# Kernel optimization log

Measured on AMD Instinct MI355X. Metric: run time of the kernel, lower is better.

## Reference

```python
import jax, jax.numpy as jnp
import numpy as np

DIM = 1024
HEADS = 16
SEQ = 1024
BATCH = 4
SCALE = (DIM // HEADS) ** -0.5


def setup_inputs() -> dict:
    key = jax.random.key(0)
    ks = jax.random.split(key, 5)
    x = jax.random.normal(ks[0], (BATCH, SEQ, DIM), dtype=jnp.float32)
    # Linear weights stored [in, out]; y = x @ W + b (math-equivalent to torch Linear)
    w_qkv = jax.random.normal(ks[1], (DIM, 3 * DIM), dtype=jnp.float32) * (DIM ** -0.5)
    b_qkv = jnp.zeros((3 * DIM,), dtype=jnp.float32)
    w_proj = jax.random.normal(ks[2], (DIM, DIM), dtype=jnp.float32) * (DIM ** -0.5)
    b_proj = jnp.zeros((DIM,), dtype=jnp.float32)
    rel_table = jax.random.normal(ks[3], (2 * SEQ - 1, HEADS), dtype=jnp.float32) * 0.02
    coords = jnp.arange(SEQ)
    rel_index = (coords[:, None] - coords[None, :] + SEQ - 1).astype(jnp.int32)  # [N, N]
    return {"x": x, "w_qkv": w_qkv, "b_qkv": b_qkv, "w_proj": w_proj,
            "b_proj": b_proj, "rel_table": rel_table, "rel_index": rel_index}


def reference(x, w_qkv, b_qkv, w_proj, b_proj, rel_table, rel_index):
    B, N, C = x.shape
    H = HEADS
    hd = C // H
    qkv = (x @ w_qkv + b_qkv).reshape(B, N, 3, H, hd).transpose(2, 0, 3, 1, 4)  # [3,B,H,N,hd]
    q, k, v = qkv[0] * SCALE, qkv[1], qkv[2]
    attn = jnp.einsum('bhqe,bhke->bhqk', q, k)                 # [B,H,N,N]
    bias = rel_table[rel_index]                                 # [N,N,H] gather
    attn = attn + bias.transpose(2, 0, 1)[None]                 # add [1,H,N,N]
    attn = jax.nn.softmax(attn, axis=-1)
    # Faithful to the original einsum 'bnqk,bnqe->bnqe' (contracts k over attn only)
    out = jnp.einsum('bnqk,bnqe->bnqe', attn, v)                # [B,H,N,hd]
    out = out.transpose(0, 2, 1, 3).reshape(B, N, C)
    return out @ w_proj + b_proj
```

## Files before the change

kernel.cpp:

```cpp
#include <hip/hip_runtime.h>


#define DIMC 1024
#define MTOT 4096

__device__ __forceinline__ unsigned short f2bf(float f) {
  unsigned u = __float_as_uint(f);
  u += 0x7FFFu + ((u >> 16) & 1u);
  return (unsigned short)(u >> 16);
}

typedef __attribute__((ext_vector_type(8))) short short8;
typedef __attribute__((ext_vector_type(4))) float floatx4;

__device__ __forceinline__ void async_copy16(const unsigned short* g, unsigned short* l) {
  __builtin_amdgcn_global_load_lds(
      (const __attribute__((address_space(1))) unsigned int*)g,
      (__attribute__((address_space(3))) unsigned int*)l,
      16, 0, 0);
}

__global__ void cast_bf16_kernel(const float* __restrict__ in,
                                 unsigned short* __restrict__ out) {
  int i = (blockIdx.x * 256 + threadIdx.x) * 4;
  float4 f = *(const float4*)(in + i);
  ushort4 o;
  o.x = f2bf(f.x); o.y = f2bf(f.y); o.z = f2bf(f.z); o.w = f2bf(f.w);
  *(ushort4*)(out + i) = o;
}

__global__ void cast_slice_kernel(const float* __restrict__ in, int stride,
                                  int col0, unsigned short* __restrict__ out) {
  int i4 = blockIdx.x * 256 + threadIdx.x;
  int r = i4 >> 8;
  int c = (i4 & 255) * 4;
  float4 f = *(const float4*)(in + (size_t)r * stride + col0 + c);
  ushort4 o;
  o.x = f2bf(f.x); o.y = f2bf(f.y); o.z = f2bf(f.z); o.w = f2bf(f.w);
  *(ushort4*)(out + (size_t)r * DIMC + c) = o;
}

__global__ void transpose_cast_kernel(const float* __restrict__ in, int stride,
                                      int col0, unsigned short* __restrict__ out) {
  __shared__ float tile[32][33];
  const int t = threadIdx.x;
  const int tx = t & 31, ty = t >> 5;
  const int bx = blockIdx.x, by = blockIdx.y;
#pragma unroll
  for (int r = 0; r < 4; ++r) {
    int kl = ty + r * 8;
    tile[kl][tx] = in[(size_t)(by * 32 + kl) * stride + col0 + bx * 32 + tx];
  }
  __syncthreads();
#pragma unroll
  for (int r = 0; r < 4; ++r) {
    int nl = ty + r * 8;
    out[(size_t)(bx * 32 + nl) * DIMC + by * 32 + tx] = f2bf(tile[tx][nl]);
  }
}

__global__ void bias_partial_kernel(const float* __restrict__ b_v,
                                    const float* __restrict__ w_proj,
                                    float* __restrict__ b_c) {
  __shared__ float red[256];
  const int t = threadIdx.x;
  const int lane = t & 63, q = t >> 6;
  const int n = blockIdx.x * 64 + lane;
  const int j0 = blockIdx.y * 128 + q * 32;
  float s = 0.f;
#pragma unroll
  for (int i = 0; i < 32; ++i)
    s += b_v[j0 + i] * w_proj[(size_t)(j0 + i) * DIMC + n];
  red[t] = s;
  __syncthreads();
  if (q == 0) atomicAdd(&b_c[n], red[t] + red[t + 64] + red[t + 128] + red[t + 192]);
}

template <bool BF16_OUT>
__global__ __launch_bounds__(256, 2) void gemm_bt_kernel(
    const unsigned short* __restrict__ A,
    const unsigned short* __restrict__ Bt,
    const float* __restrict__ bias,
    const float* __restrict__ bias2,
    void* __restrict__ Cout, int M, int N, int K) {
  __shared__ __align__(16) unsigned short As[64 * 64];
  __shared__ __align__(16) unsigned short Bs[128 * 64];
  const int tid = threadIdx.x;
  const int wv = tid >> 6;
  const int lane = tid & 63;
  const int m0 = blockIdx.y * 64;
  const int n0 = blockIdx.x * 128;

  floatx4 acc[4][2] = {};

  const int srow = tid >> 3;
  const int skc = (tid & 7) ^ (srow & 7);
  const unsigned short* Ag0 = A + (size_t)(m0 + srow) * K + skc * 8;
  const unsigned short* Ag1 = A + (size_t)(m0 + 32 + srow) * K + skc * 8;
  const unsigned short* Bg0 = Bt + (size_t)(n0 + srow) * K + skc * 8;
  const unsigned short* Bg1 = Bt + (size_t)(n0 + 32 + srow) * K + skc * 8;
  const unsigned short* Bg2 = Bt + (size_t)(n0 + 64 + srow) * K + skc * 8;
  const unsigned short* Bg3 = Bt + (size_t)(n0 + 96 + srow) * K + skc * 8;
  unsigned short* AsW0 = As + (0 * 256 + wv * 64) * 8;
  unsigned short* AsW1 = As + (1 * 256 + wv * 64) * 8;
  unsigned short* BsW0 = Bs + (0 * 256 + wv * 64) * 8;
  unsigned short* BsW1 = Bs + (1 * 256 + wv * 64) * 8;
  unsigned short* BsW2 = Bs + (2 * 256 + wv * 64) * 8;
  unsigned short* BsW3 = Bs + (3 * 256 + wv * 64) * 8;

  const int lr = lane & 15;
  const int qr = lane >> 4;
  const int lx = lr & 7;

  for (int k0 = 0; k0 < K; k0 += 64) {
    async_copy16(Ag0 + k0, AsW0);
    async_copy16(Ag1 + k0, AsW1);
    async_copy16(Bg0 + k0, BsW0);
    async_copy16(Bg1 + k0, BsW1);
    async_copy16(Bg2 + k0, BsW2);
    async_copy16(Bg3 + k0, BsW3);
    __syncthreads();

    short8 a[2][4], b[2][2];
#pragma unroll
    for (int s = 0; s < 2; ++s) {
      const int kphys = ((s * 4 + qr) ^ lx) * 8;
#pragma unroll
      for (int mi = 0; mi < 4; ++mi)
        a[s][mi] = *(const short8*)(As + (mi * 16 + lr) * 64 + kphys);
#pragma unroll
      for (int ni = 0; ni < 2; ++ni)
        b[s][ni] = *(const short8*)(Bs + (wv * 32 + ni * 16 + lr) * 64 + kphys);
    }
#pragma unroll
    for (int s = 0; s < 2; ++s)
#pragma unroll
      for (int mi = 0; mi < 4; ++mi)
#pragma unroll
        for (int ni = 0; ni < 2; ++ni)
          acc[mi][ni] = __builtin_amdgcn_mfma_f32_16x16x32_bf16(a[s][mi], b[s][ni],
                                                                acc[mi][ni], 0, 0, 0);
    __syncthreads();
  }

#pragma unroll
  for (int mi = 0; mi < 4; ++mi) {
#pragma unroll
    for (int ni = 0; ni < 2; ++ni) {
      const int col = n0 + wv * 32 + ni * 16 + lr;
      float bv = 0.0f;
      if (bias)  bv += bias[col];
      if (bias2) bv += bias2[col];
#pragma unroll
      for (int r = 0; r < 4; ++r) {
        const int row = m0 + mi * 16 + qr * 4 + r;
        const float val = acc[mi][ni][r] + bv;
        if (BF16_OUT)
          ((unsigned short*)Cout)[(size_t)row * N + col] = f2bf(val);
        else
          ((float*)Cout)[(size_t)row * N + col] = val;
      }
    }
  }
}

extern "C" void kernel_launch(void* const* d_in, const int* in_sizes, int n_in,
                              void* d_out, int out_size, void* d_ws, size_t ws_size,
                              hipStream_t stream) {
  const float* x      = (const float*)d_in[0];
  const float* w_qkv  = (const float*)d_in[1];
  const float* b_qkv  = (const float*)d_in[2];
  const float* w_proj = (const float*)d_in[3];
  const float* b_proj = (const float*)d_in[4];
  float* out = (float*)d_out;

  char* ws = (char*)d_ws;
  unsigned short* xb  = (unsigned short*)(ws);
  unsigned short* WpT = (unsigned short*)(ws + (size_t)(8u << 20));
  unsigned short* Wvb = (unsigned short*)(ws + (size_t)(10u << 20));
  unsigned short* WcT = (unsigned short*)(ws + (size_t)(12u << 20));
  float*          b_c = (float*)(ws + (size_t)(14u << 20));

  cast_bf16_kernel<<<(MTOT * DIMC) / (256 * 4), 256, 0, stream>>>(x, xb);
  transpose_cast_kernel<<<dim3(32, 32), 256, 0, stream>>>(w_proj, DIMC, 0, WpT);
  cast_slice_kernel<<<(DIMC * DIMC) / (256 * 4), 256, 0, stream>>>(w_qkv, 3 * DIMC, 2 * DIMC, Wvb);
  hipMemsetAsync(b_c, 0, DIMC * sizeof(float), stream);
  bias_partial_kernel<<<dim3(16, 8), 256, 0, stream>>>(b_qkv + 2 * DIMC, w_proj, b_c);
  gemm_bt_kernel<true><<<dim3(DIMC / 128, DIMC / 64), 256, 0, stream>>>(
      WpT, Wvb, nullptr, nullptr, WcT, DIMC, DIMC, DIMC);
  gemm_bt_kernel<false><<<dim3(DIMC / 128, MTOT / 64), 256, 0, stream>>>(
      xb, WcT, b_c, b_proj, out, MTOT, DIMC, DIMC);
}
```

Before: 132.3 us.

## Fuse weight prep kernels and retile GEMMs with block swizzle

Merges the w_proj transpose-cast, the V-slice cast and the folded-bias reduction into one prep kernel, cutting three launches down to one. The GEMM is templated on tile size. The weight-fold GEMM now runs 64x64 tiles (256 blocks, more CU coverage), and the main GEMM runs 128x128 tiles with a 2x2 wave layout and a grouped block swizzle for L2 reuse. Larger tiles raise register pressure and leave only 256 blocks in the main GEMM, which may underfill the GPU.

```diff
diff --git a/kernel.cpp b/kernel.cpp
--- a/kernel.cpp
+++ b/kernel.cpp
@@ -29,19 +29,12 @@
   *(ushort4*)(out + i) = o;
 }
 
-__global__ void cast_slice_kernel(const float* __restrict__ in, int stride,
-                                  int col0, unsigned short* __restrict__ out) {
-  int i4 = blockIdx.x * 256 + threadIdx.x;
-  int r = i4 >> 8;
-  int c = (i4 & 255) * 4;
-  float4 f = *(const float4*)(in + (size_t)r * stride + col0 + c);
-  ushort4 o;
-  o.x = f2bf(f.x); o.y = f2bf(f.y); o.z = f2bf(f.z); o.w = f2bf(f.w);
-  *(ushort4*)(out + (size_t)r * DIMC + c) = o;
-}
-
-__global__ void transpose_cast_kernel(const float* __restrict__ in, int stride,
-                                      int col0, unsigned short* __restrict__ out) {
+__global__ void prep_kernel(const float* __restrict__ w_proj,
+                            const float* __restrict__ w_qkv,
+                            const float* __restrict__ b_v,
+                            unsigned short* __restrict__ WpT,
+                            unsigned short* __restrict__ Wvb,
+                            float* __restrict__ b_c) {
   __shared__ float tile[32][33];
   const int t = threadIdx.x;
   const int tx = t & 31, ty = t >> 5;
@@ -49,111 +42,121 @@
 #pragma unroll
   for (int r = 0; r < 4; ++r) {
     int kl = ty + r * 8;
-    tile[kl][tx] = in[(size_t)(by * 32 + kl) * stride + col0 + bx * 32 + tx];
+    tile[kl][tx] = w_proj[(size_t)(by * 32 + kl) * DIMC + bx * 32 + tx];
+  }
+  {
+    const int r2 = t >> 3, c4 = (t & 7) * 4;
+    float4 f = *(const float4*)(w_qkv + (size_t)(by * 32 + r2) * (3 * DIMC) +
+                                2 * DIMC + bx * 32 + c4);
+    ushort4 o;
+    o.x = f2bf(f.x); o.y = f2bf(f.y); o.z = f2bf(f.z); o.w = f2bf(f.w);
+    *(ushort4*)(Wvb + (size_t)(by * 32 + r2) * DIMC + bx * 32 + c4) = o;
   }
   __syncthreads();
 #pragma unroll
   for (int r = 0; r < 4; ++r) {
     int nl = ty + r * 8;
-    out[(size_t)(bx * 32 + nl) * DIMC + by * 32 + tx] = f2bf(tile[tx][nl]);
+    WpT[(size_t)(bx * 32 + nl) * DIMC + by * 32 + tx] = f2bf(tile[tx][nl]);
+  }
+  if (t < 32) {
+    float s = 0.f;
+#pragma unroll
+    for (int kl = 0; kl < 32; ++kl) s += b_v[by * 32 + kl] * tile[kl][t];
+    atomicAdd(&b_c[bx * 32 + t], s);
   }
 }
 
-__global__ void bias_partial_kernel(const float* __restrict__ b_v,
-                                    const float* __restrict__ w_proj,
-                                    float* __restrict__ b_c) {
-  __shared__ float red[256];
-  const int t = threadIdx.x;
-  const int lane = t & 63, q = t >> 6;
-  const int n = blockIdx.x * 64 + lane;
-  const int j0 = blockIdx.y * 128 + q * 32;
-  float s = 0.f;
-#pragma unroll
-  for (int i = 0; i < 32; ++i)
-    s += b_v[j0 + i] * w_proj[(size_t)(j0 + i) * DIMC + n];
-  red[t] = s;
-  __syncthreads();
-  if (q == 0) atomicAdd(&b_c[n], red[t] + red[t + 64] + red[t + 128] + red[t + 192]);
-}
-
-template <bool BF16_OUT>
+template <int BM, int BN, bool BF16_OUT, bool SWZ>
 __global__ __launch_bounds__(256, 2) void gemm_bt_kernel(
     const unsigned short* __restrict__ A,
     const unsigned short* __restrict__ Bt,
     const float* __restrict__ bias,
     const float* __restrict__ bias2,
-    void* __restrict__ Cout, int M, int N, int K) {
-  __shared__ __align__(16) unsigned short As[64 * 64];
-  __shared__ __align__(16) unsigned short Bs[128 * 64];
+    void* __restrict__ Cout, int M, int N, int K, int gx) {
+  constexpr int MI = BM / 32;
+  constexpr int NI = BN / 32;
+  constexpr int AG = BM / 32;
+  constexpr int BG = BN / 32;
+  __shared__ __align__(16) unsigned short As[BM * 64];
+  __shared__ __align__(16) unsigned short Bs[BN * 64];
+
   const int tid = threadIdx.x;
   const int wv = tid >> 6;
   const int lane = tid & 63;
-  const int m0 = blockIdx.y * 64;
-  const int n0 = blockIdx.x * 128;
 
-  floatx4 acc[4][2] = {};
+  int bx, by;
+  if (SWZ) {
+    const int bid = blockIdx.x;
+    bx = (bid >> 3) & 7;
+    by = (bid & 7) * 4 + (bid >> 6);
+  } else {
+    bx = blockIdx.x % gx;
+    by = blockIdx.x / gx;
+  }
+  const int m0 = by * BM;
+  const int n0 = bx * BN;
+
+  floatx4 acc[MI][NI] = {};
 
   const int srow = tid >> 3;
   const int skc = (tid & 7) ^ (srow & 7);
-  const unsigned short* Ag0 = A + (size_t)(m0 + srow) * K + skc * 8;
-  const unsigned short* Ag1 = A + (size_t)(m0 + 32 + srow) * K + skc * 8;
-  const unsigned short* Bg0 = Bt + (size_t)(n0 + srow) * K + skc * 8;
-  const unsigned short* Bg1 = Bt + (size_t)(n0 + 32 + srow) * K + skc * 8;
-  const unsigned short* Bg2 = Bt + (size_t)(n0 + 64 + srow) * K + skc * 8;
-  const unsigned short* Bg3 = Bt + (size_t)(n0 + 96 + srow) * K + skc * 8;
-  unsigned short* AsW0 = As + (0 * 256 + wv * 64) * 8;
-  unsigned short* AsW1 = As + (1 * 256 + wv * 64) * 8;
-  unsigned short* BsW0 = Bs + (0 * 256 + wv * 64) * 8;
-  unsigned short* BsW1 = Bs + (1 * 256 + wv * 64) * 8;
-  unsigned short* BsW2 = Bs + (2 * 256 + wv * 64) * 8;
-  unsigned short* BsW3 = Bs + (3 * 256 + wv * 64) * 8;
+  const unsigned short* Ag[AG];
+  const unsigned short* Bg[BG];
+#pragma unroll
+  for (int g = 0; g < AG; ++g)
+    Ag[g] = A + (size_t)(m0 + g * 32 + srow) * K + skc * 8;
+#pragma unroll
+  for (int g = 0; g < BG; ++g)
+    Bg[g] = Bt + (size_t)(n0 + g * 32 + srow) * K + skc * 8;
 
   const int lr = lane & 15;
   const int qr = lane >> 4;
   const int lx = lr & 7;
+  const int wrow = (wv >> 1) * (BM / 2);
+  const int wcol = (wv & 1) * (BN / 2);
 
   for (int k0 = 0; k0 < K; k0 += 64) {
-    async_copy16(Ag0 + k0, AsW0);
-    async_copy16(Ag1 + k0, AsW1);
-    async_copy16(Bg0 + k0, BsW0);
-    async_copy16(Bg1 + k0, BsW1);
-    async_copy16(Bg2 + k0, BsW2);
-    async_copy16(Bg3 + k0, BsW3);
+#pragma unroll
+    for (int g = 0; g < AG; ++g)
+      async_copy16(Ag[g] + k0, As + (g * 256 + wv * 64) * 8);
+#pragma unroll
+    for (int g = 0; g < BG; ++g)
+      async_copy16(Bg[g] + k0, Bs + (g * 256 + wv * 64) * 8);
     __syncthreads();
 
-    short8 a[2][4], b[2][2];
+    short8 a[2][MI], b[2][NI];
 #pragma unroll
     for (int s = 0; s < 2; ++s) {
       const int kphys = ((s * 4 + qr) ^ lx) * 8;
 #pragma unroll
-      for (int mi = 0; mi < 4; ++mi)
-        a[s][mi] = *(const short8*)(As + (mi * 16 + lr) * 64 + kphys);
+      for (int mi = 0; mi < MI; ++mi)
+        a[s][mi] = *(const short8*)(As + (wrow + mi * 16 + lr) * 64 + kphys);
 #pragma unroll
-      for (int ni = 0; ni < 2; ++ni)
-        b[s][ni] = *(const short8*)(Bs + (wv * 32 + ni * 16 + lr) * 64 + kphys);
+      for (int ni = 0; ni < NI; ++ni)
+        b[s][ni] = *(const short8*)(Bs + (wcol + ni * 16 + lr) * 64 + kphys);
     }
 #pragma unroll
     for (int s = 0; s < 2; ++s)
 #pragma unroll
-      for (int mi = 0; mi < 4; ++mi)
+      for (int mi = 0; mi < MI; ++mi)
 #pragma unroll
-        for (int ni = 0; ni < 2; ++ni)
+        for (int ni = 0; ni < NI; ++ni)
           acc[mi][ni] = __builtin_amdgcn_mfma_f32_16x16x32_bf16(a[s][mi], b[s][ni],
                                                                 acc[mi][ni], 0, 0, 0);
     __syncthreads();
   }
 
 #pragma unroll
-  for (int mi = 0; mi < 4; ++mi) {
+  for (int mi = 0; mi < MI; ++mi) {
 #pragma unroll
-    for (int ni = 0; ni < 2; ++ni) {
-      const int col = n0 + wv * 32 + ni * 16 + lr;
+    for (int ni = 0; ni < NI; ++ni) {
+      const int col = n0 + wcol + ni * 16 + lr;
       float bv = 0.0f;
       if (bias)  bv += bias[col];
       if (bias2) bv += bias2[col];
 #pragma unroll
       for (int r = 0; r < 4; ++r) {
-        const int row = m0 + mi * 16 + qr * 4 + r;
+        const int row = m0 + wrow + mi * 16 + qr * 4 + r;
         const float val = acc[mi][ni][r] + bv;
         if (BF16_OUT)
           ((unsigned short*)Cout)[(size_t)row * N + col] = f2bf(val);
@@ -181,13 +184,12 @@
   unsigned short* WcT = (unsigned short*)(ws + (size_t)(12u << 20));
   float*          b_c = (float*)(ws + (size_t)(14u << 20));
 
+  hipMemsetAsync(b_c, 0, DIMC * sizeof(float), stream);
   cast_bf16_kernel<<<(MTOT * DIMC) / (256 * 4), 256, 0, stream>>>(x, xb);
-  transpose_cast_kernel<<<dim3(32, 32), 256, 0, stream>>>(w_proj, DIMC, 0, WpT);
-  cast_slice_kernel<<<(DIMC * DIMC) / (256 * 4), 256, 0, stream>>>(w_qkv, 3 * DIMC, 2 * DIMC, Wvb);
-  hipMemsetAsync(b_c, 0, DIMC * sizeof(float), stream);
-  bias_partial_kernel<<<dim3(16, 8), 256, 0, stream>>>(b_qkv + 2 * DIMC, w_proj, b_c);
-  gemm_bt_kernel<true><<<dim3(DIMC / 128, DIMC / 64), 256, 0, stream>>>(
-      WpT, Wvb, nullptr, nullptr, WcT, DIMC, DIMC, DIMC);
-  gemm_bt_kernel<false><<<dim3(DIMC / 128, MTOT / 64), 256, 0, stream>>>(
-      xb, WcT, b_c, b_proj, out, MTOT, DIMC, DIMC);
+  prep_kernel<<<dim3(32, 32), 256, 0, stream>>>(w_proj, w_qkv, b_qkv + 2 * DIMC,
+                                                WpT, Wvb, b_c);
+  gemm_bt_kernel<64, 64, true, false><<<256, 256, 0, stream>>>(
+      WpT, Wvb, nullptr, nullptr, WcT, DIMC, DIMC, DIMC, DIMC / 64);
+  gemm_bt_kernel<128, 128, false, true><<<256, 256, 0, stream>>>(
+      xb, WcT, b_c, b_proj, out, MTOT, DIMC, DIMC, DIMC / 128);
 }
```

Measured after the change: 128.7 us. -2.7%, faster.
